# Performance work log

Hardware: AMD Instinct MI355X
Metric: run time of the kernel (lower is better)

## Reference

```python
import jax, jax.numpy as jnp
import numpy as np

HEADS = 12
HEAD_SIZE = 64
HIDDEN = 768
NEG = 1e12


def _rope_sincos(n, d, dtype):
    # SinusoidalPositionEmbedding merge_mode='zero': [n, d] interleaved (sin, cos)
    pos = jnp.arange(n, dtype=jnp.float32)
    inv = jnp.power(10000.0, -2.0 * jnp.arange(d // 2, dtype=jnp.float32) / d)
    ang = pos[:, None] * inv[None, :]                       # [n, d/2]
    sin, cos = jnp.sin(ang), jnp.cos(ang)
    # repeat_interleave(2) of sinusoidal[...,1::2] (cos) and [...,::2] (sin)
    cos_pos = jnp.repeat(cos, 2, axis=-1).astype(dtype)     # [n, d]
    sin_pos = jnp.repeat(sin, 2, axis=-1).astype(dtype)
    return sin_pos[None, :, None, :], cos_pos[None, :, None, :]  # [1,n,1,d]


def _rotate_half_interleaved(x):
    # stack([-x[...,1::2], x[...,::2]], -1).reshape(x.shape): (-x1,x0,-x3,x2,...)
    x2 = jnp.stack([-x[..., 1::2], x[..., ::2]], axis=-1)
    return x2.reshape(x.shape)


def setup_inputs() -> dict:
    key = jax.random.key(0)
    kx, kw, kb = jax.random.split(key, 3)
    B, N = 8, 1024
    x = jax.random.normal(kx, (B, N, HIDDEN), dtype=jnp.float32)
    W = jax.random.normal(kw, (HIDDEN, 2 * HEADS * HEAD_SIZE), dtype=jnp.float32) * 0.02
    b = jnp.zeros((2 * HEADS * HEAD_SIZE,), dtype=jnp.float32)
    mask = jnp.ones((B, N), dtype=jnp.float32)
    return {"x": x, "W": W, "b": b, "mask": mask}


def reference(x, W, b, mask):
    B, N, D = x.shape
    proj = jnp.einsum('bnd,de->bne', x, W) + b              # [B,N,2*H*hs]
    proj = proj.reshape(B, N, HEADS, 2 * HEAD_SIZE)
    qw, kw = proj[..., :HEAD_SIZE], proj[..., HEAD_SIZE:]   # [B,N,H,hs]

    sin_pos, cos_pos = _rope_sincos(N, HEAD_SIZE, qw.dtype)
    qw = qw * cos_pos + _rotate_half_interleaved(qw) * sin_pos
    kw = kw * cos_pos + _rotate_half_interleaved(kw) * sin_pos

    logits = jnp.einsum('bmhd,bnhd->bhmn', qw, kw)          # [B,H,N,N]

    # sequence masking on query axis (ndim-2) and key axis (ndim-1)
    mq = mask[:, None, :, None]
    mk = mask[:, None, None, :]
    logits = logits * mq + NEG * (mq - 1.0)
    logits = logits * mk + NEG * (mk - 1.0)

    # strict lower-triangular mask (diagonal=-1)
    tril = jnp.tril(jnp.ones((N, N), dtype=logits.dtype), k=-1)
    logits = logits - tril * NEG
    return logits / (HEAD_SIZE ** 0.5)
```

## Files before the change

kernel.cpp:

```cpp
#include <hip/hip_runtime.h>

typedef _Float16 f16x8 __attribute__((ext_vector_type(8)));
typedef _Float16 f16x4 __attribute__((ext_vector_type(4)));
typedef float    f32x4 __attribute__((ext_vector_type(4)));

#define NH    12
#define HS    64
#define HID   768
#define EDIM  1536
#define NSEQ  1024
#define BSZ   8
#define MTOT  8192

#define XH_OFF 0u
#define WT_OFF 12582912u
#define QH_OFF 14942208u
#define KH_OFF 27525120u
#define ST_OFF 40108032u
#define CT_OFF 40239104u

__device__ __forceinline__ void gl_lds16(const void* g, void* l) {
  __builtin_amdgcn_global_load_lds(
      (const __attribute__((address_space(1))) void*)g,
      (__attribute__((address_space(3))) void*)l, 16, 0, 0);
}

__global__ void prep_kernel(const float* __restrict__ x, const float* __restrict__ W,
                            _Float16* __restrict__ xh, _Float16* __restrict__ wt,
                            float* __restrict__ st, float* __restrict__ ct) {
  int tid = blockIdx.x * blockDim.x + threadIdx.x;
  int T = gridDim.x * blockDim.x;
  const float4* x4 = (const float4*)x;
  f16x4* xh4 = (f16x4*)xh;
  for (int i = tid; i < (MTOT * HID / 4); i += T) {
    float4 v = x4[i];
    f16x4 h;
    h.x = (_Float16)v.x; h.y = (_Float16)v.y; h.z = (_Float16)v.z; h.w = (_Float16)v.w;
    xh4[i] = h;
  }
  for (int i = tid; i < EDIM * HID; i += T) {
    int e = i / HID;
    int k = i - e * HID;
    wt[i] = (_Float16)W[(size_t)k * EDIM + e];
  }
  for (int i = tid; i < NSEQ * 32; i += T) {
    int pos = i >> 5, fi = i & 31;
    float inv = powf(10000.0f, -(float)fi * (1.0f / 32.0f));
    float ang = (float)pos * inv;
    st[i] = sinf(ang);
    ct[i] = cosf(ang);
  }
}

__global__ __launch_bounds__(256, 2) void gemm1_kernel(
    const _Float16* __restrict__ xh, const _Float16* __restrict__ wt,
    const float* __restrict__ bias, const float* __restrict__ st,
    const float* __restrict__ ct,
    _Float16* __restrict__ qh, _Float16* __restrict__ kh) {
  __shared__ __align__(16) _Float16 Ab[128 * 32];
  __shared__ __align__(16) _Float16 Bb[128 * 32];
  const int tid = threadIdx.x;
  const int w = tid >> 6, l = tid & 63;
  const int wm = w & 1, wn = w >> 1;
  const int m0 = blockIdx.x * 128, e0 = blockIdx.y * 128;

  const int rsub = l >> 2;
  const int swz = (l & 3) ^ ((l >> 2) & 3) ^ (l >> 4);

  f32x4 acc[4][4] = {};

  for (int kt = 0; kt < HID; kt += 32) {
#pragma unroll
    for (int j = 0; j < 2; ++j) {
      int ch = w * 2 + j;
      gl_lds16(xh + (size_t)(m0 + ch * 16 + rsub) * HID + kt + swz * 8, &Ab[ch * 512]);
    }
#pragma unroll
    for (int j = 0; j < 2; ++j) {
      int ch = w * 2 + j;
      gl_lds16(wt + (size_t)(e0 + ch * 16 + rsub) * HID + kt + swz * 8, &Bb[ch * 512]);
    }
    __syncthreads();
    f16x8 af[4], bf[4];
#pragma unroll
    for (int mi = 0; mi < 4; ++mi)
      af[mi] = *(const f16x8*)&Ab[(wm * 64 + mi * 16 + (l & 15)) * 32 + swz * 8];
#pragma unroll
    for (int ni = 0; ni < 4; ++ni)
      bf[ni] = *(const f16x8*)&Bb[(wn * 64 + ni * 16 + (l & 15)) * 32 + swz * 8];
#pragma unroll
    for (int mi = 0; mi < 4; ++mi)
#pragma unroll
      for (int ni = 0; ni < 4; ++ni)
        acc[mi][ni] = __builtin_amdgcn_mfma_f32_16x16x32_f16(af[mi], bf[ni], acc[mi][ni], 0, 0, 0);
    __syncthreads();
  }

#pragma unroll
  for (int ni = 0; ni < 4; ++ni) {
    const int e = e0 + wn * 64 + ni * 16 + (l & 15);
    const float bv = bias[e];
    const int ia = (e & 63) >> 1;
    const int hh = e >> 7;
    const int cc = e & 127;
    _Float16* const dst = (cc < 64) ? qh : kh;
    const int d = cc & 63;
    const float sgn = (e & 1) ? 1.0f : -1.0f;
#pragma unroll
    for (int mi = 0; mi < 4; ++mi) {
#pragma unroll
      for (int j = 0; j < 4; ++j) {
        const int m = m0 + wm * 64 + mi * 16 + ((l >> 4) << 2) + j;
        const int bidx = m >> 10;
        const int pos = m & 1023;
        float v = acc[mi][ni][j] + bv;
        float p = __shfl_xor(v, 1);
        const float cs = ct[pos * 32 + ia];
        const float sn = st[pos * 32 + ia];
        float ov = v * cs + sgn * p * sn;
        dst[(((size_t)bidx * NH + hh) * NSEQ + pos) * HS + d] = (_Float16)ov;
      }
    }
  }
}

__global__ __launch_bounds__(256, 2) void scores_kernel(
    const _Float16* __restrict__ qh, const _Float16* __restrict__ kh,
    const float* __restrict__ mask, float* __restrict__ out) {
  __shared__ __align__(16) _Float16 Qb[128 * 64];
  __shared__ __align__(16) _Float16 Kb[128 * 64];
  const int tid = threadIdx.x;
  const int w = tid >> 6, l = tid & 63;
  const int wm = w & 1, wn = w >> 1;
  const int bh = blockIdx.z;
  const int bb = bh / NH;
  const int m0 = blockIdx.y * 128, n0 = blockIdx.x * 128;
  const _Float16* qbase = qh + (size_t)bh * NSEQ * HS + (size_t)m0 * HS;
  const _Float16* kbase = kh + (size_t)bh * NSEQ * HS + (size_t)n0 * HS;

#pragma unroll
  for (int j = 0; j < 4; ++j) {
    const int r = w * 32 + j * 8 + (l >> 3);
    const int c = (l & 7) ^ ((l >> 3) & 7);
    gl_lds16(qbase + r * 64 + c * 8, &Qb[w * 2048 + j * 512]);
    gl_lds16(kbase + r * 64 + c * 8, &Kb[w * 2048 + j * 512]);
  }
  __syncthreads();

  f32x4 acc[4][4] = {};
#pragma unroll
  for (int ks = 0; ks < 2; ++ks) {
    const int cl = ks * 4 + (l >> 4);
    f16x8 af[4], bf[4];
#pragma unroll
    for (int mi = 0; mi < 4; ++mi) {
      const int r = wm * 64 + mi * 16 + (l & 15);
      af[mi] = *(const f16x8*)&Qb[r * 64 + (cl ^ (l & 7)) * 8];
    }
#pragma unroll
    for (int ni = 0; ni < 4; ++ni) {
      const int r = wn * 64 + ni * 16 + (l & 15);
      bf[ni] = *(const f16x8*)&Kb[r * 64 + (cl ^ (l & 7)) * 8];
    }
#pragma unroll
    for (int mi = 0; mi < 4; ++mi)
#pragma unroll
      for (int ni = 0; ni < 4; ++ni)
        acc[mi][ni] = __builtin_amdgcn_mfma_f32_16x16x32_f16(af[mi], bf[ni], acc[mi][ni], 0, 0, 0);
  }

  const float NEGC = 1000000000000.0f;
  float mkv[4];
  int nn[4];
#pragma unroll
  for (int ni = 0; ni < 4; ++ni) {
    nn[ni] = n0 + wn * 64 + ni * 16 + (l & 15);
    mkv[ni] = mask[bb * NSEQ + nn[ni]];
  }
#pragma unroll
  for (int mi = 0; mi < 4; ++mi) {
#pragma unroll
    for (int j = 0; j < 4; ++j) {
      const int m = m0 + wm * 64 + mi * 16 + ((l >> 4) << 2) + j;
      const float mq = mask[bb * NSEQ + m];
      const size_t rowbase = ((size_t)bh * NSEQ + m) * NSEQ;
#pragma unroll
      for (int ni = 0; ni < 4; ++ni) {
        float v = acc[mi][ni][j];
        v = v * mq + NEGC * (mq - 1.0f);
        v = v * mkv[ni] + NEGC * (mkv[ni] - 1.0f);
        if (nn[ni] < m) v -= NEGC;
        out[rowbase + nn[ni]] = v * 0.125f;
      }
    }
  }
}

extern "C" void kernel_launch(void* const* d_in, const int* in_sizes, int n_in,
                              void* d_out, int out_size, void* d_ws, size_t ws_size,
                              hipStream_t stream) {
  const float* x    = (const float*)d_in[0];
  const float* W    = (const float*)d_in[1];
  const float* bias = (const float*)d_in[2];
  const float* mask = (const float*)d_in[3];
  float* out = (float*)d_out;
  char* ws = (char*)d_ws;

  _Float16* xh = (_Float16*)(ws + XH_OFF);
  _Float16* wt = (_Float16*)(ws + WT_OFF);
  _Float16* qh = (_Float16*)(ws + QH_OFF);
  _Float16* kh = (_Float16*)(ws + KH_OFF);
  float* st = (float*)(ws + ST_OFF);
  float* ct = (float*)(ws + CT_OFF);

  prep_kernel<<<2048, 256, 0, stream>>>(x, W, xh, wt, st, ct);

  dim3 g1(MTOT / 128, EDIM / 128);
  gemm1_kernel<<<g1, 256, 0, stream>>>(xh, wt, bias, st, ct, qh, kh);

  dim3 g2(NSEQ / 128, NSEQ / 128, BSZ * NH);
  scores_kernel<<<g2, 256, 0, stream>>>(qh, kh, mask, out);
}
```

Baseline: 476.4 us.

## Double-buffer GEMM LDS tiles, tile W transpose via LDS, interleave sin/cos table

The projection GEMM now keeps two LDS stages, so the next K tile's global-to-LDS loads are issued before the current tile is computed, and one barrier per iteration is removed. The prep kernel gives 288 blocks to an LDS-tiled transpose of W, making its strided, uncoalesced reads coalesced, while the remaining blocks convert x. The sin and cos tables are interleaved into one float2 array so the RoPE epilogue does one load instead of two. The cost is double the LDS use in the GEMM and a static split of blocks in prep.

```diff
diff --git a/kernel.cpp b/kernel.cpp
--- a/kernel.cpp
+++ b/kernel.cpp
@@ -16,8 +16,7 @@
 #define WT_OFF 12582912u
 #define QH_OFF 14942208u
 #define KH_OFF 27525120u
-#define ST_OFF 40108032u
-#define CT_OFF 40239104u
+#define CS_OFF 40108032u
 
 __device__ __forceinline__ void gl_lds16(const void* g, void* l) {
   __builtin_amdgcn_global_load_lds(
@@ -27,38 +26,55 @@
 
 __global__ void prep_kernel(const float* __restrict__ x, const float* __restrict__ W,
                             _Float16* __restrict__ xh, _Float16* __restrict__ wt,
-                            float* __restrict__ st, float* __restrict__ ct) {
-  int tid = blockIdx.x * blockDim.x + threadIdx.x;
-  int T = gridDim.x * blockDim.x;
-  const float4* x4 = (const float4*)x;
-  f16x4* xh4 = (f16x4*)xh;
-  for (int i = tid; i < (MTOT * HID / 4); i += T) {
-    float4 v = x4[i];
-    f16x4 h;
-    h.x = (_Float16)v.x; h.y = (_Float16)v.y; h.z = (_Float16)v.z; h.w = (_Float16)v.w;
-    xh4[i] = h;
-  }
-  for (int i = tid; i < EDIM * HID; i += T) {
-    int e = i / HID;
-    int k = i - e * HID;
-    wt[i] = (_Float16)W[(size_t)k * EDIM + e];
-  }
-  for (int i = tid; i < NSEQ * 32; i += T) {
-    int pos = i >> 5, fi = i & 31;
-    float inv = powf(10000.0f, -(float)fi * (1.0f / 32.0f));
-    float ang = (float)pos * inv;
-    st[i] = sinf(ang);
-    ct[i] = cosf(ang);
+                            float* __restrict__ cst) {
+  const int b = blockIdx.x;
+  const int t = threadIdx.x;
+  if (b < 288) {
+    __shared__ _Float16 lt[64][66];
+    const int te = b % 24, tk = b / 24;
+    const int e0t = te * 64, k0t = tk * 64;
+#pragma unroll
+    for (int i = 0; i < 16; ++i) {
+      const int idx = i * 256 + t;
+      const int kl = idx >> 6, el = idx & 63;
+      lt[el][kl] = (_Float16)W[(size_t)(k0t + kl) * EDIM + e0t + el];
+    }
+    __syncthreads();
+#pragma unroll
+    for (int i = 0; i < 4; ++i) {
+      const int idx = i * 256 + t;
+      const int el = idx >> 4, kl4 = (idx & 15) * 4;
+      f16x4 v;
+      v.x = lt[el][kl4]; v.y = lt[el][kl4 + 1]; v.z = lt[el][kl4 + 2]; v.w = lt[el][kl4 + 3];
+      *(f16x4*)&wt[(size_t)(e0t + el) * HID + k0t + kl4] = v;
+    }
+  } else {
+    const int tid = (b - 288) * 256 + t;
+    const int T = (gridDim.x - 288) * 256;
+    const float4* x4 = (const float4*)x;
+    f16x4* xh4 = (f16x4*)xh;
+    for (int i = tid; i < (MTOT * HID / 4); i += T) {
+      float4 v = x4[i];
+      f16x4 h;
+      h.x = (_Float16)v.x; h.y = (_Float16)v.y; h.z = (_Float16)v.z; h.w = (_Float16)v.w;
+      xh4[i] = h;
+    }
+    for (int i = tid; i < NSEQ * 32; i += T) {
+      const int pos = i >> 5, fi = i & 31;
+      const float inv = powf(10000.0f, -(float)fi * (1.0f / 32.0f));
+      const float ang = (float)pos * inv;
+      cst[i * 2]     = cosf(ang);
+      cst[i * 2 + 1] = sinf(ang);
+    }
   }
 }
 
 __global__ __launch_bounds__(256, 2) void gemm1_kernel(
     const _Float16* __restrict__ xh, const _Float16* __restrict__ wt,
-    const float* __restrict__ bias, const float* __restrict__ st,
-    const float* __restrict__ ct,
+    const float* __restrict__ bias, const float* __restrict__ cst,
     _Float16* __restrict__ qh, _Float16* __restrict__ kh) {
-  __shared__ __align__(16) _Float16 Ab[128 * 32];
-  __shared__ __align__(16) _Float16 Bb[128 * 32];
+  __shared__ __align__(16) _Float16 Ab[2][128 * 32];
+  __shared__ __align__(16) _Float16 Bb[2][128 * 32];
   const int tid = threadIdx.x;
   const int w = tid >> 6, l = tid & 63;
   const int wm = w & 1, wn = w >> 1;
@@ -69,33 +85,42 @@
 
   f32x4 acc[4][4] = {};
 
-  for (int kt = 0; kt < HID; kt += 32) {
+  auto stage = [&](int buf, int kt) {
 #pragma unroll
     for (int j = 0; j < 2; ++j) {
-      int ch = w * 2 + j;
-      gl_lds16(xh + (size_t)(m0 + ch * 16 + rsub) * HID + kt + swz * 8, &Ab[ch * 512]);
-    }
-#pragma unroll
-    for (int j = 0; j < 2; ++j) {
-      int ch = w * 2 + j;
-      gl_lds16(wt + (size_t)(e0 + ch * 16 + rsub) * HID + kt + swz * 8, &Bb[ch * 512]);
-    }
-    __syncthreads();
+      const int ch = w * 2 + j;
+      gl_lds16(xh + (size_t)(m0 + ch * 16 + rsub) * HID + kt + swz * 8, &Ab[buf][ch * 512]);
+      gl_lds16(wt + (size_t)(e0 + ch * 16 + rsub) * HID + kt + swz * 8, &Bb[buf][ch * 512]);
+    }
+  };
+
+  auto compute = [&](int buf) {
     f16x8 af[4], bf[4];
 #pragma unroll
     for (int mi = 0; mi < 4; ++mi)
-      af[mi] = *(const f16x8*)&Ab[(wm * 64 + mi * 16 + (l & 15)) * 32 + swz * 8];
+      af[mi] = *(const f16x8*)&Ab[buf][(wm * 64 + mi * 16 + (l & 15)) * 32 + swz * 8];
 #pragma unroll
     for (int ni = 0; ni < 4; ++ni)
-      bf[ni] = *(const f16x8*)&Bb[(wn * 64 + ni * 16 + (l & 15)) * 32 + swz * 8];
+      bf[ni] = *(const f16x8*)&Bb[buf][(wn * 64 + ni * 16 + (l & 15)) * 32 + swz * 8];
 #pragma unroll
     for (int mi = 0; mi < 4; ++mi)
 #pragma unroll
       for (int ni = 0; ni < 4; ++ni)
         acc[mi][ni] = __builtin_amdgcn_mfma_f32_16x16x32_f16(af[mi], bf[ni], acc[mi][ni], 0, 0, 0);
+  };
+
+  stage(0, 0);
+  __syncthreads();
+  int cur = 0;
+  for (int kt = 32; kt < HID; kt += 32) {
+    stage(cur ^ 1, kt);
+    compute(cur);
     __syncthreads();
-  }
-
+    cur ^= 1;
+  }
+  compute(cur);
+
+  const float2* cst2 = (const float2*)cst;
 #pragma unroll
   for (int ni = 0; ni < 4; ++ni) {
     const int e = e0 + wn * 64 + ni * 16 + (l & 15);
@@ -115,9 +140,8 @@
         const int pos = m & 1023;
         float v = acc[mi][ni][j] + bv;
         float p = __shfl_xor(v, 1);
-        const float cs = ct[pos * 32 + ia];
-        const float sn = st[pos * 32 + ia];
-        float ov = v * cs + sgn * p * sn;
+        const float2 cs = cst2[pos * 32 + ia];
+        float ov = v * cs.x + sgn * p * cs.y;
         dst[(((size_t)bidx * NH + hh) * NSEQ + pos) * HS + d] = (_Float16)ov;
       }
     }
@@ -210,13 +234,12 @@
   _Float16* wt = (_Float16*)(ws + WT_OFF);
   _Float16* qh = (_Float16*)(ws + QH_OFF);
   _Float16* kh = (_Float16*)(ws + KH_OFF);
-  float* st = (float*)(ws + ST_OFF);
-  float* ct = (float*)(ws + CT_OFF);
-
-  prep_kernel<<<2048, 256, 0, stream>>>(x, W, xh, wt, st, ct);
+  float* cst = (float*)(ws + CS_OFF);
+
+  prep_kernel<<<2048, 256, 0, stream>>>(x, W, xh, wt, cst);
 
   dim3 g1(MTOT / 128, EDIM / 128);
-  gemm1_kernel<<<g1, 256, 0, stream>>>(xh, wt, bias, st, ct, qh, kh);
+  gemm1_kernel<<<g1, 256, 0, stream>>>(xh, wt, bias, cst, qh, kh);
 
   dim3 g2(NSEQ / 128, NSEQ / 128, BSZ * NH);
   scores_kernel<<<g2, 256, 0, stream>>>(qh, kh, mask, out);
```

Result: faster. 466.0 us (-2.2%).
